# Optimization experiments

Hardware: AMD Instinct MI355X
Metric: run time of the kernel (lower is better)

The kernel has to match this reference:

```python
import jax, jax.numpy as jnp
import numpy as np

V, E, H, B, S = 32000, 512, 1024, 128, 512
NEG = -1e9


def setup_inputs() -> dict:
    key = jax.random.key(0)
    ks = jax.random.split(key, 12)
    s = 0.02
    return {
        "previous_word": jax.random.randint(ks[0], (B, 1), 0, V),
        "h_0": jax.random.normal(ks[1], (B, H), jnp.float32),
        "c_0": jax.random.normal(ks[2], (B, H), jnp.float32),
        "ctx": jax.random.normal(ks[3], (B, S, H), jnp.float32),
        "ctx_mask": jnp.zeros((B, S), dtype=bool),
        "emb": jax.random.normal(ks[4], (V, E), jnp.float32) * s,
        "W_ih": jax.random.normal(ks[5], (4 * H, E), jnp.float32) * s,
        "W_hh": jax.random.normal(ks[6], (4 * H, H), jnp.float32) * s,
        "b_ih": jnp.zeros((4 * H,), jnp.float32),
        "b_hh": jnp.zeros((4 * H,), jnp.float32),
        "W_in": jax.random.normal(ks[7], (H, H), jnp.float32) * s,
        "W_out": jax.random.normal(ks[8], (H, 2 * H), jnp.float32) * s,
        "W_dec": jax.random.normal(ks[9], (V, H), jnp.float32) * s,
        "b_dec": jnp.zeros((V,), jnp.float32),
    }


def reference(previous_word, h_0, c_0, ctx, ctx_mask, emb, W_ih, W_hh, b_ih, b_hh, W_in, W_out, W_dec, b_dec):
    # embedding lookup + squeeze; dropout is identity in eval mode
    x = emb[previous_word[:, 0]]                       # [B, E]
    # LSTMCell: gate order i, f, g, o (PyTorch convention)
    gates = x @ W_ih.T + b_ih + h_0 @ W_hh.T + b_hh    # [B, 4H]
    i, f, g, o = jnp.split(gates, 4, axis=1)
    i = jax.nn.sigmoid(i)
    f = jax.nn.sigmoid(f)
    g = jnp.tanh(g)
    o = jax.nn.sigmoid(o)
    c_1 = f * c_0 + i * g
    h_1 = o * jnp.tanh(c_1)
    # SoftDotAttention
    target = h_1 @ W_in.T                               # [B, H]
    attn = jnp.einsum('bsh,bh->bs', ctx, target)        # [B, S]
    attn = jnp.where(ctx_mask, NEG, attn)
    alpha = jax.nn.softmax(attn, axis=1)
    weighted = jnp.einsum('bs,bsh->bh', alpha, ctx)     # [B, H]
    h_tilde = jnp.tanh(jnp.concatenate([weighted, h_1], axis=1) @ W_out.T)
    logit = h_tilde @ W_dec.T + b_dec                   # [B, V]
    return (h_1, c_1, alpha, logit)
```

## Files before the change

kernel.cpp:

```cpp
#include <hip/hip_runtime.h>
#include <hip/hip_bf16.h>
#include <cstdint>

#define NEG_BIG (-1.0e9f)

typedef __attribute__((ext_vector_type(8))) short short8_t;
typedef __attribute__((ext_vector_type(4))) float f32x4;

typedef __attribute__((address_space(1))) const unsigned int gu32_t;
typedef __attribute__((address_space(3))) unsigned int lu32_t;

__device__ __forceinline__ short f2bf(float x) {
  union { float f; unsigned u; } v; v.f = x;
  unsigned r = v.u + 0x7fffu + ((v.u >> 16) & 1u);
  return (short)(r >> 16);
}
__device__ __forceinline__ float sigmoidf_(float x) { return 1.0f / (1.0f + __expf(-x)); }

__device__ __forceinline__ void lds_barrier() {
  asm volatile("s_waitcnt lgkmcnt(0)\n\ts_barrier" ::: "memory");
}
__device__ __forceinline__ void block_barrier() {
  asm volatile("" ::: "memory");
  __builtin_amdgcn_s_barrier();
  asm volatile("" ::: "memory");
}

__launch_bounds__(256, 2)
__global__ void k_gates(const int* __restrict__ prev, const float* __restrict__ emb,
                        const float* __restrict__ h0,
                        const float* __restrict__ W_ih, const float* __restrict__ W_hh,
                        const float* __restrict__ b_ih, const float* __restrict__ b_hh,
                        const float* __restrict__ c0,
                        float* __restrict__ h1_out, float* __restrict__ c1_out,
                        short* __restrict__ A3) {
  __shared__ __align__(16) short lA[2][64 * 64];
  __shared__ __align__(16) short lW[2][64 * 64];
  const int tid = threadIdx.x;
  const int wid = tid >> 6, l = tid & 63, l15 = l & 15, khalf = l >> 4;
  const int hb = blockIdx.x;
  const int mrow0 = blockIdx.y * 64;

  const int arow = tid >> 2;
  const int apart = tid & 3;
  const int aswz = (arow & 7) << 4;
  const int bA = mrow0 + arow;
  const int pv = prev[bA];
  const float* embrow = emb + (size_t)pv * 512 + apart * 16;
  const float* h0row = h0 + (size_t)bA * 1024 + apart * 16;

  int wrow_[4], wkq_[4];
  const float* wih_[4];
  const float* whh_[4];
#pragma unroll
  for (int j = 0; j < 4; ++j) {
    int idx = j * 1024 + tid * 4;
    int n = idx >> 6;
    wkq_[j] = idx & 63;
    wrow_[j] = n;
    int grow = (n >> 4) * 1024 + hb * 16 + (n & 15);
    wih_[j] = W_ih + (size_t)grow * 512;
    whh_[j] = W_hh + (size_t)grow * 1024;
  }

  f32x4 acc[4];
#pragma unroll
  for (int r = 0; r < 4; ++r) acc[r] = (f32x4){0.f, 0.f, 0.f, 0.f};

  float4 aF[4], wR[4];
  auto stage_regs = [&](int k0) {
    const float* asrc = (k0 < 512) ? (embrow + k0) : (h0row + (k0 - 512));
#pragma unroll
    for (int q = 0; q < 4; ++q) aF[q] = *(const float4*)(asrc + q * 4);
#pragma unroll
    for (int j = 0; j < 4; ++j) {
      int kg = k0 + wkq_[j];
      wR[j] = (kg < 512) ? *(const float4*)(wih_[j] + kg)
                         : *(const float4*)(whh_[j] + (kg - 512));
    }
  };
  auto write_lds = [&](int buf) {
    char* drow = (char*)lA[buf] + arow * 128;
#pragma unroll
    for (int q = 0; q < 2; ++q) {
      short8_t s;
      s[0] = f2bf(aF[2 * q].x); s[1] = f2bf(aF[2 * q].y);
      s[2] = f2bf(aF[2 * q].z); s[3] = f2bf(aF[2 * q].w);
      s[4] = f2bf(aF[2 * q + 1].x); s[5] = f2bf(aF[2 * q + 1].y);
      s[6] = f2bf(aF[2 * q + 1].z); s[7] = f2bf(aF[2 * q + 1].w);
      *(short8_t*)(drow + ((apart * 32 + q * 16) ^ aswz)) = s;
    }
#pragma unroll
    for (int j = 0; j < 4; ++j) {
      short4 h4;
      h4.x = f2bf(wR[j].x); h4.y = f2bf(wR[j].y); h4.z = f2bf(wR[j].z); h4.w = f2bf(wR[j].w);
      *(short4*)((char*)lW[buf] + wrow_[j] * 128 + ((wkq_[j] * 2) ^ ((wrow_[j] & 7) << 4))) = h4;
    }
  };
  auto compute = [&](int buf) {
#pragma unroll
    for (int ks = 0; ks < 2; ++ks) {
      const int ubyte = ks * 64 + khalf * 16;
      const int nrow = wid * 16 + l15;
      short8_t bfrag = *(const short8_t*)((char*)lW[buf] + nrow * 128 + (ubyte ^ ((nrow & 7) << 4)));
#pragma unroll
      for (int r = 0; r < 4; ++r) {
        const int mrow = r * 16 + l15;
        short8_t afrag = *(const short8_t*)((char*)lA[buf] + mrow * 128 + (ubyte ^ ((mrow & 7) << 4)));
        acc[r] = __builtin_amdgcn_mfma_f32_16x16x32_bf16(afrag, bfrag, acc[r], 0, 0, 0);
      }
    }
  };

  stage_regs(0);
  write_lds(0);
  for (int t = 0; t < 24; ++t) {
    const int cur = t & 1;
    if (t + 1 < 24) stage_regs((t + 1) << 6);
    lds_barrier();
    compute(cur);
    if (t + 1 < 24) write_lds(cur ^ 1);
  }

  lds_barrier();
  float* gbuf = (float*)&lA[0][0];
#pragma unroll
  for (int r = 0; r < 4; ++r)
#pragma unroll
    for (int e = 0; e < 4; ++e)
      gbuf[wid * 1024 + (r * 16 + khalf * 4 + e) * 16 + l15] = acc[r][e];
  __syncthreads();
#pragma unroll
  for (int q = 0; q < 4; ++q) {
    int idx = q * 256 + tid;
    int hloc = idx & 15, mloc = idx >> 4;
    int b = mrow0 + mloc;
    int hh = hb * 16 + hloc;
    float iv = gbuf[0 + mloc * 16 + hloc] + b_ih[hh] + b_hh[hh];
    float fv = gbuf[1024 + mloc * 16 + hloc] + b_ih[1024 + hh] + b_hh[1024 + hh];
    float gv = gbuf[2048 + mloc * 16 + hloc] + b_ih[2048 + hh] + b_hh[2048 + hh];
    float ov = gbuf[3072 + mloc * 16 + hloc] + b_ih[3072 + hh] + b_hh[3072 + hh];
    float c1 = sigmoidf_(fv) * c0[(size_t)b * 1024 + hh] + sigmoidf_(iv) * tanhf(gv);
    float h1 = sigmoidf_(ov) * tanhf(c1);
    c1_out[(size_t)b * 1024 + hh] = c1;
    h1_out[(size_t)b * 1024 + hh] = h1;
    A3[(size_t)b * 2048 + 1024 + hh] = f2bf(h1);
  }
}

template <int MB, int WN, int EPI>
__launch_bounds__(256, 2)
__global__ void k_gemm(const short* __restrict__ A, int lda,
                       const float* __restrict__ Wa, int ldwa, int Ka,
                       const float* __restrict__ Wb, int ldwb, int Ktot,
                       const float* __restrict__ bias0, const float* __restrict__ bias1,
                       float* __restrict__ outF, short* __restrict__ outB, int ldo,
                       int kstride, size_t pstride) {
  constexpr int BN = WN * 16;
  constexpr int MREP = (MB == 128) ? 2 * WN : 1;
  constexpr int AU = MB / 32;
  constexpr int WLOADS = (BN * 64) / 1024;
  __shared__ __align__(16) short lA[2][MB * 64];
  __shared__ __align__(16) short lW[2][BN * 64];
  const int kc = blockIdx.z;
  A += (size_t)kc * kstride;
  Wa += (size_t)kc * kstride;
  if (outF) outF += (size_t)kc * pstride;
  const int tid = threadIdx.x;
  const int wid = tid >> 6, l = tid & 63, l15 = l & 15, khalf = l >> 4;
  const int nblk = blockIdx.x;
  const int mrow0 = blockIdx.y * MB;
  const int m_wave = (WN == 1) ? wid * (MB / 4) : 0;
  const int nb_local = (WN == 4) ? wid * 16 : 0;

  const int arow = (MB == 128) ? (tid >> 1) : (tid >> 2);
  const int apart = (MB == 128) ? (tid & 1) : (tid & 3);
  const int abase = apart * (AU * 16);
  const int aswz = (arow & 7) << 4;
  const short* Arow = A + (size_t)(mrow0 + arow) * lda + apart * (AU * 8);

  int wn_[WLOADS], wkq_[WLOADS];
#pragma unroll
  for (int j = 0; j < WLOADS; ++j) {
    int idx = j * 1024 + tid * 4;
    wn_[j] = idx >> 6;
    wkq_[j] = idx & 63;
  }

  f32x4 acc[MREP];
#pragma unroll
  for (int r = 0; r < MREP; ++r) acc[r] = (f32x4){0.f, 0.f, 0.f, 0.f};

  short8_t aR[AU];
  float4 wR[WLOADS];

  auto stage_regs = [&](int k0) {
#pragma unroll
    for (int q = 0; q < AU; ++q) aR[q] = *(const short8_t*)(Arow + k0 + q * 8);
#pragma unroll
    for (int j = 0; j < WLOADS; ++j) {
      int kg = k0 + wkq_[j];
      const float* p = (kg < Ka) ? (Wa + (size_t)(nblk * BN + wn_[j]) * ldwa + kg)
                                 : (Wb + (size_t)(nblk * BN + wn_[j]) * ldwb + (kg - Ka));
      wR[j] = *(const float4*)p;
    }
  };
  auto write_lds = [&](int buf) {
    char* drow = (char*)lA[buf] + arow * 128;
#pragma unroll
    for (int q = 0; q < AU; ++q)
      *(short8_t*)(drow + ((abase + q * 16) ^ aswz)) = aR[q];
#pragma unroll
    for (int j = 0; j < WLOADS; ++j) {
      short4 h4;
      h4.x = f2bf(wR[j].x); h4.y = f2bf(wR[j].y); h4.z = f2bf(wR[j].z); h4.w = f2bf(wR[j].w);
      *(short4*)((char*)lW[buf] + wn_[j] * 128 + ((wkq_[j] * 2) ^ ((wn_[j] & 7) << 4))) = h4;
    }
  };
  auto compute = [&](int buf) {
#pragma unroll
    for (int ks = 0; ks < 2; ++ks) {
      const int ubyte = ks * 64 + khalf * 16;
      const int nrow = nb_local + l15;
      short8_t bfrag = *(const short8_t*)((char*)lW[buf] + nrow * 128 + (ubyte ^ ((nrow & 7) << 4)));
#pragma unroll
      for (int r = 0; r < MREP; ++r) {
        const int mrow = m_wave + r * 16 + l15;
        short8_t afrag = *(const short8_t*)((char*)lA[buf] + mrow * 128 + (ubyte ^ ((mrow & 7) << 4)));
        acc[r] = __builtin_amdgcn_mfma_f32_16x16x32_bf16(afrag, bfrag, acc[r], 0, 0, 0);
      }
    }
  };

  const int NT = Ktot >> 6;
  stage_regs(0);
  write_lds(0);
  for (int t = 0; t < NT; ++t) {
    const int cur = t & 1;
    if (t + 1 < NT) stage_regs((t + 1) << 6);
    lds_barrier();
    compute(cur);
    if (t + 1 < NT) write_lds(cur ^ 1);
  }

  const int n = nblk * BN + nb_local + l15;
  float bias = 0.f;
  if (bias0) bias = bias0[n];
  if (bias1) bias += bias1[n];
#pragma unroll
  for (int r = 0; r < MREP; ++r) {
    int mb = mrow0 + m_wave + r * 16 + khalf * 4;
#pragma unroll
    for (int e = 0; e < 4; ++e) {
      float v = acc[r][e] + bias;
      if (EPI == 1) {
        outB[(size_t)(mb + e) * ldo + n] = f2bf(tanhf(v));
      } else {
        outF[(size_t)(mb + e) * ldo + n] = v;
      }
    }
  }
}

__launch_bounds__(256, 2)
__global__ void k_attn(const float* __restrict__ ctx, const float* __restrict__ tp,
                       const unsigned char* __restrict__ mask,
                       float* __restrict__ scores, float* __restrict__ part) {
  __shared__ __align__(16) float lds[2][8 * 1024];
  __shared__ float sml[8];
  const int b = blockIdx.x >> 2, chunk = blockIdx.x & 3;
  const int tid = threadIdx.x;
  const int wid = tid >> 6, l = tid & 63;
  float4 t4[4], w4[4];
#pragma unroll
  for (int j = 0; j < 4; ++j) {
    float4 a = {0.f, 0.f, 0.f, 0.f};
#pragma unroll
    for (int p = 0; p < 4; ++p) {
      const float4 v = *(const float4*)(tp + (size_t)p * 131072 + (size_t)b * 1024 + j * 256 + l * 4);
      a.x += v.x; a.y += v.y; a.z += v.z; a.w += v.w;
    }
    t4[j] = a;
    w4[j].x = 0.f; w4[j].y = 0.f; w4[j].z = 0.f; w4[j].w = 0.f;
  }
  float m = -INFINITY, lsum = 0.f;
  const int s0 = chunk * 128;
  const float* cb = ctx + ((size_t)b * 512 + s0) * 1024;
  const unsigned char* mk = mask + (size_t)b * 512 + s0;

  auto stage = [&](int buf, int tt) {
    const char* src = (const char*)(cb + (size_t)tt * 8192);
    char* dst = (char*)&lds[buf][0];
#pragma unroll
    for (int i = 0; i < 8; ++i) {
      const int off = i * 4096 + tid * 16;
      __builtin_amdgcn_global_load_lds((gu32_t*)(src + off), (lu32_t*)(dst + off), 16, 0, 0);
    }
  };

  stage(0, 0);
  int buf = 0;
  for (int t = 0; t < 16; ++t) {
    if (t < 15) {
      stage(buf ^ 1, t + 1);
      asm volatile("s_waitcnt vmcnt(8)" ::: "memory");
    } else {
      asm volatile("s_waitcnt vmcnt(0)" ::: "memory");
    }
    block_barrier();
#pragma unroll
    for (int rr = 0; rr < 2; ++rr) {
      const int r = wid * 2 + rr;
      const float* row = &lds[buf][r * 1024];
      float4 c0 = *(const float4*)(row + l * 4);
      float4 c1 = *(const float4*)(row + 256 + l * 4);
      float4 c2 = *(const float4*)(row + 512 + l * 4);
      float4 c3 = *(const float4*)(row + 768 + l * 4);
      float p = c0.x * t4[0].x + c0.y * t4[0].y + c0.z * t4[0].z + c0.w * t4[0].w +
                c1.x * t4[1].x + c1.y * t4[1].y + c1.z * t4[1].z + c1.w * t4[1].w +
                c2.x * t4[2].x + c2.y * t4[2].y + c2.z * t4[2].z + c2.w * t4[2].w +
                c3.x * t4[3].x + c3.y * t4[3].y + c3.z * t4[3].z + c3.w * t4[3].w;
#pragma unroll
      for (int off = 32; off > 0; off >>= 1) p += __shfl_xor(p, off);
      const int sg = t * 8 + r;
      if (mk[sg]) p = NEG_BIG;
      if (l == 0) scores[(size_t)b * 512 + s0 + sg] = p;
      float mn = fmaxf(m, p);
      float scale = __expf(m - mn);
      float e = __expf(p - mn);
      lsum = lsum * scale + e;
      w4[0].x = w4[0].x * scale + e * c0.x; w4[0].y = w4[0].y * scale + e * c0.y;
      w4[0].z = w4[0].z * scale + e * c0.z; w4[0].w = w4[0].w * scale + e * c0.w;
      w4[1].x = w4[1].x * scale + e * c1.x; w4[1].y = w4[1].y * scale + e * c1.y;
      w4[1].z = w4[1].z * scale + e * c1.z; w4[1].w = w4[1].w * scale + e * c1.w;
      w4[2].x = w4[2].x * scale + e * c2.x; w4[2].y = w4[2].y * scale + e * c2.y;
      w4[2].z = w4[2].z * scale + e * c2.z; w4[2].w = w4[2].w * scale + e * c2.w;
      w4[3].x = w4[3].x * scale + e * c3.x; w4[3].y = w4[3].y * scale + e * c3.y;
      w4[3].z = w4[3].z * scale + e * c3.z; w4[3].w = w4[3].w * scale + e * c3.w;
      m = mn;
    }
    block_barrier();
    buf ^= 1;
  }

  float* cbuf = &lds[0][0];
#pragma unroll
  for (int j = 0; j < 4; ++j) *(float4*)(cbuf + wid * 1024 + j * 256 + l * 4) = w4[j];
  if (l == 0) { sml[wid] = m; sml[4 + wid] = lsum; }
  __syncthreads();
  const float M = fmaxf(fmaxf(sml[0], sml[1]), fmaxf(sml[2], sml[3]));
  const float sc0 = __expf(sml[0] - M), sc1 = __expf(sml[1] - M);
  const float sc2 = __expf(sml[2] - M), sc3 = __expf(sml[3] - M);
  const float L = sml[4] * sc0 + sml[5] * sc1 + sml[6] * sc2 + sml[7] * sc3;
  const float4 v0 = *(const float4*)(cbuf + 0 * 1024 + tid * 4);
  const float4 v1 = *(const float4*)(cbuf + 1 * 1024 + tid * 4);
  const float4 v2 = *(const float4*)(cbuf + 2 * 1024 + tid * 4);
  const float4 v3 = *(const float4*)(cbuf + 3 * 1024 + tid * 4);
  float4 o;
  o.x = v0.x * sc0 + v1.x * sc1 + v2.x * sc2 + v3.x * sc3;
  o.y = v0.y * sc0 + v1.y * sc1 + v2.y * sc2 + v3.y * sc3;
  o.z = v0.z * sc0 + v1.z * sc1 + v2.z * sc2 + v3.z * sc3;
  o.w = v0.w * sc0 + v1.w * sc1 + v2.w * sc2 + v3.w * sc3;
  float* pp = part + ((size_t)b * 4 + chunk) * 1028;
  *(float4*)(pp + tid * 4) = o;
  if (tid == 0) { pp[1024] = M; pp[1025] = L; }
}

__launch_bounds__(256, 2)
__global__ void k_wgemm(const short* __restrict__ A3, const float* __restrict__ part,
                        const float* __restrict__ W_out, float* __restrict__ wp) {
  __shared__ __align__(16) short lA[2][128 * 64];
  __shared__ __align__(16) short lW[2][16 * 64];
  const int kc = blockIdx.z, nblk = blockIdx.x;
  const int tid = threadIdx.x;
  const int wid = tid >> 6, l = tid & 63, l15 = l & 15, khalf = l >> 4;
  const int arow = tid >> 1, apart = tid & 1;
  const int aswz = (arow & 7) << 4;
  const bool wpath = (kc < 4);

  const int colbase = kc * 256 + apart * 32;
  const short* ArowB = A3 + (size_t)arow * 2048 + colbase;
  const float* ps = part + (size_t)arow * 4 * 1028;
  const float* pr0 = ps + colbase;
  const float* pr1 = ps + 1028 + colbase;
  const float* pr2 = ps + 2056 + colbase;
  const float* pr3 = ps + 3084 + colbase;
  float coef0 = 0.f, coef1 = 0.f, coef2 = 0.f, coef3 = 0.f;
  if (wpath) {
    float m0 = ps[1024], l0 = ps[1025], m1 = ps[1028 + 1024], l1 = ps[1028 + 1025];
    float m2 = ps[2056 + 1024], l2 = ps[2056 + 1025], m3 = ps[3084 + 1024], l3 = ps[3084 + 1025];
    float M = fmaxf(fmaxf(m0, m1), fmaxf(m2, m3));
    float s0 = __expf(m0 - M), s1 = __expf(m1 - M), s2 = __expf(m2 - M), s3 = __expf(m3 - M);
    float inv = 1.0f / (l0 * s0 + l1 * s1 + l2 * s2 + l3 * s3);
    coef0 = s0 * inv; coef1 = s1 * inv; coef2 = s2 * inv; coef3 = s3 * inv;
  }

  const int wn = (tid * 4) >> 6, wkq = (tid * 4) & 63;
  const float* wrow = W_out + (size_t)(nblk * 16 + wn) * 2048 + kc * 256;

  f32x4 acc[2];
  acc[0] = (f32x4){0.f, 0.f, 0.f, 0.f};
  acc[1] = (f32x4){0.f, 0.f, 0.f, 0.f};
  float4 aC[8];
  short8_t aB[4];
  float4 wR;

  auto stage_regs = [&](int k0) {
    if (wpath) {
#pragma unroll
      for (int q = 0; q < 8; ++q) {
        const float4 v0 = *(const float4*)(pr0 + k0 + q * 4);
        const float4 v1 = *(const float4*)(pr1 + k0 + q * 4);
        const float4 v2 = *(const float4*)(pr2 + k0 + q * 4);
        const float4 v3 = *(const float4*)(pr3 + k0 + q * 4);
        aC[q].x = coef0 * v0.x + coef1 * v1.x + coef2 * v2.x + coef3 * v3.x;
        aC[q].y = coef0 * v0.y + coef1 * v1.y + coef2 * v2.y + coef3 * v3.y;
        aC[q].z = coef0 * v0.z + coef1 * v1.z + coef2 * v2.z + coef3 * v3.z;
        aC[q].w = coef0 * v0.w + coef1 * v1.w + coef2 * v2.w + coef3 * v3.w;
      }
    } else {
#pragma unroll
      for (int q = 0; q < 4; ++q) aB[q] = *(const short8_t*)(ArowB + k0 + q * 8);
    }
    wR = *(const float4*)(wrow + k0 + wkq);
  };
  auto write_lds = [&](int buf) {
    char* drow = (char*)lA[buf] + arow * 128;
    if (wpath) {
#pragma unroll
      for (int q2 = 0; q2 < 4; ++q2) {
        short8_t s;
        s[0] = f2bf(aC[2 * q2].x); s[1] = f2bf(aC[2 * q2].y);
        s[2] = f2bf(aC[2 * q2].z); s[3] = f2bf(aC[2 * q2].w);
        s[4] = f2bf(aC[2 * q2 + 1].x); s[5] = f2bf(aC[2 * q2 + 1].y);
        s[6] = f2bf(aC[2 * q2 + 1].z); s[7] = f2bf(aC[2 * q2 + 1].w);
        *(short8_t*)(drow + ((apart * 64 + q2 * 16) ^ aswz)) = s;
      }
    } else {
#pragma unroll
      for (int q = 0; q < 4; ++q)
        *(short8_t*)(drow + ((apart * 64 + q * 16) ^ aswz)) = aB[q];
    }
    short4 h4;
    h4.x = f2bf(wR.x); h4.y = f2bf(wR.y); h4.z = f2bf(wR.z); h4.w = f2bf(wR.w);
    *(short4*)((char*)lW[buf] + wn * 128 + ((wkq * 2) ^ ((wn & 7) << 4))) = h4;
  };
  auto compute = [&](int buf) {
#pragma unroll
    for (int ks = 0; ks < 2; ++ks) {
      const int ubyte = ks * 64 + khalf * 16;
      short8_t bfrag = *(const short8_t*)((char*)lW[buf] + l15 * 128 + (ubyte ^ ((l15 & 7) << 4)));
#pragma unroll
      for (int r = 0; r < 2; ++r) {
        const int mrow = wid * 32 + r * 16 + l15;
        short8_t afrag = *(const short8_t*)((char*)lA[buf] + mrow * 128 + (ubyte ^ ((mrow & 7) << 4)));
        acc[r] = __builtin_amdgcn_mfma_f32_16x16x32_bf16(afrag, bfrag, acc[r], 0, 0, 0);
      }
    }
  };

  stage_regs(0);
  write_lds(0);
  for (int t = 0; t < 4; ++t) {
    const int cur = t & 1;
    if (t + 1 < 4) stage_regs((t + 1) << 6);
    lds_barrier();
    compute(cur);
    if (t + 1 < 4) write_lds(cur ^ 1);
  }

  const int n = nblk * 16 + l15;
  float* out = wp + (size_t)kc * 131072;
#pragma unroll
  for (int r = 0; r < 2; ++r) {
    int mb = wid * 32 + r * 16 + khalf * 4;
#pragma unroll
    for (int e = 0; e < 4; ++e)
      out[(size_t)(mb + e) * 1024 + n] = acc[r][e];
  }
}

__global__ void k_fin2(const float* __restrict__ wp, const float* __restrict__ part,
                       const float* __restrict__ scores, short* __restrict__ ht,
                       float* __restrict__ alpha) {
  int t = blockIdx.x * 256 + threadIdx.x;
  float s = 0.f;
#pragma unroll
  for (int p = 0; p < 8; ++p) s += wp[(size_t)p * 131072 + t];
  ht[t] = f2bf(tanhf(s));
  if (t < 65536) {
    int b = t >> 9, si = t & 511;
    const float* ps = part + (size_t)b * 4 * 1028;
    float m0 = ps[1024], l0 = ps[1025], m1 = ps[1028 + 1024], l1 = ps[1028 + 1025];
    float m2 = ps[2056 + 1024], l2 = ps[2056 + 1025], m3 = ps[3084 + 1024], l3 = ps[3084 + 1025];
    float M = fmaxf(fmaxf(m0, m1), fmaxf(m2, m3));
    float L = l0 * __expf(m0 - M) + l1 * __expf(m1 - M) + l2 * __expf(m2 - M) +
              l3 * __expf(m3 - M);
    alpha[t] = __expf(scores[(size_t)b * 512 + si] - M) / L;
  }
}

extern "C" void kernel_launch(void* const* d_in, const int* in_sizes, int n_in,
                              void* d_out, int out_size, void* d_ws, size_t ws_size,
                              hipStream_t stream) {
  const int* prev = (const int*)d_in[0];
  const float* h0 = (const float*)d_in[1];
  const float* c0 = (const float*)d_in[2];
  const float* ctx = (const float*)d_in[3];
  const unsigned char* mask = (const unsigned char*)d_in[4];
  const float* emb = (const float*)d_in[5];
  const float* W_ih = (const float*)d_in[6];
  const float* W_hh = (const float*)d_in[7];
  const float* b_ih = (const float*)d_in[8];
  const float* b_hh = (const float*)d_in[9];
  const float* W_in = (const float*)d_in[10];
  const float* W_out = (const float*)d_in[11];
  const float* W_dec = (const float*)d_in[12];
  const float* b_dec = (const float*)d_in[13];

  float* out_h1 = (float*)d_out;
  float* out_c1 = out_h1 + 128 * 1024;
  float* out_alpha = out_c1 + 128 * 1024;
  float* out_logit = out_alpha + 128 * 512;

  char* ws = (char*)d_ws;
  short* A3 = (short*)(ws + 0x000000);
  float* scores = (float*)(ws + 0x100000);
  float* tp = (float*)(ws + 0x200000);
  float* part = (float*)(ws + 0x400000);
  float* wp = (float*)(ws + 0x700000);
  short* htilde = (short*)(ws + 0xB00000);

  k_gates<<<dim3(64, 2), 256, 0, stream>>>(prev, emb, h0, W_ih, W_hh, b_ih, b_hh, c0,
                                           out_h1, out_c1, A3);
  k_gemm<128, 1, 0><<<dim3(64, 1, 4), 256, 0, stream>>>(
      A3 + 1024, 2048, W_in, 1024, 1 << 30, W_in, 1024, 256, nullptr, nullptr, tp, nullptr,
      1024, 256, (size_t)131072);
  k_attn<<<512, 256, 0, stream>>>(ctx, tp, mask, scores, part);
  k_wgemm<<<dim3(64, 1, 8), 256, 0, stream>>>(A3, part, W_out, wp);
  k_fin2<<<512, 256, 0, stream>>>(wp, part, scores, htilde, out_alpha);
  k_gemm<128, 4, 0><<<dim3(500, 1, 1), 256, 0, stream>>>(
      htilde, 1024, W_dec, 1024, 1024, W_dec, 1024, 1024, b_dec, nullptr, out_logit, nullptr,
      32000, 0, 0);
}
```

Baseline: 144.1 us.

## Split fused LSTM gate kernel into pack, generic GEMM, and pointwise kernels

Replaces the fused k_gates kernel, which ran on a 64x2 grid, with three steps. A packing kernel writes the bf16 [emb|h0] activations, the generic k_gemm then runs over 256 blocks to produce fp32 gates, and a pointwise LSTM kernel computes c1 and h1. The goal is to spread the gate GEMM across more blocks and CUs so the weight streaming parallelises better. In exchange it adds two extra launches and round-trips the gates and the packed activations through global memory.

```diff
diff --git a/kernel.cpp b/kernel.cpp
--- a/kernel.cpp
+++ b/kernel.cpp
@@ -26,126 +26,13 @@
   asm volatile("" ::: "memory");
 }
 
-__launch_bounds__(256, 2)
-__global__ void k_gates(const int* __restrict__ prev, const float* __restrict__ emb,
-                        const float* __restrict__ h0,
-                        const float* __restrict__ W_ih, const float* __restrict__ W_hh,
-                        const float* __restrict__ b_ih, const float* __restrict__ b_hh,
-                        const float* __restrict__ c0,
-                        float* __restrict__ h1_out, float* __restrict__ c1_out,
-                        short* __restrict__ A3) {
-  __shared__ __align__(16) short lA[2][64 * 64];
-  __shared__ __align__(16) short lW[2][64 * 64];
-  const int tid = threadIdx.x;
-  const int wid = tid >> 6, l = tid & 63, l15 = l & 15, khalf = l >> 4;
-  const int hb = blockIdx.x;
-  const int mrow0 = blockIdx.y * 64;
-
-  const int arow = tid >> 2;
-  const int apart = tid & 3;
-  const int aswz = (arow & 7) << 4;
-  const int bA = mrow0 + arow;
-  const int pv = prev[bA];
-  const float* embrow = emb + (size_t)pv * 512 + apart * 16;
-  const float* h0row = h0 + (size_t)bA * 1024 + apart * 16;
-
-  int wrow_[4], wkq_[4];
-  const float* wih_[4];
-  const float* whh_[4];
-#pragma unroll
-  for (int j = 0; j < 4; ++j) {
-    int idx = j * 1024 + tid * 4;
-    int n = idx >> 6;
-    wkq_[j] = idx & 63;
-    wrow_[j] = n;
-    int grow = (n >> 4) * 1024 + hb * 16 + (n & 15);
-    wih_[j] = W_ih + (size_t)grow * 512;
-    whh_[j] = W_hh + (size_t)grow * 1024;
-  }
-
-  f32x4 acc[4];
-#pragma unroll
-  for (int r = 0; r < 4; ++r) acc[r] = (f32x4){0.f, 0.f, 0.f, 0.f};
-
-  float4 aF[4], wR[4];
-  auto stage_regs = [&](int k0) {
-    const float* asrc = (k0 < 512) ? (embrow + k0) : (h0row + (k0 - 512));
-#pragma unroll
-    for (int q = 0; q < 4; ++q) aF[q] = *(const float4*)(asrc + q * 4);
-#pragma unroll
-    for (int j = 0; j < 4; ++j) {
-      int kg = k0 + wkq_[j];
-      wR[j] = (kg < 512) ? *(const float4*)(wih_[j] + kg)
-                         : *(const float4*)(whh_[j] + (kg - 512));
-    }
-  };
-  auto write_lds = [&](int buf) {
-    char* drow = (char*)lA[buf] + arow * 128;
-#pragma unroll
-    for (int q = 0; q < 2; ++q) {
-      short8_t s;
-      s[0] = f2bf(aF[2 * q].x); s[1] = f2bf(aF[2 * q].y);
-      s[2] = f2bf(aF[2 * q].z); s[3] = f2bf(aF[2 * q].w);
-      s[4] = f2bf(aF[2 * q + 1].x); s[5] = f2bf(aF[2 * q + 1].y);
-      s[6] = f2bf(aF[2 * q + 1].z); s[7] = f2bf(aF[2 * q + 1].w);
-      *(short8_t*)(drow + ((apart * 32 + q * 16) ^ aswz)) = s;
-    }
-#pragma unroll
-    for (int j = 0; j < 4; ++j) {
-      short4 h4;
-      h4.x = f2bf(wR[j].x); h4.y = f2bf(wR[j].y); h4.z = f2bf(wR[j].z); h4.w = f2bf(wR[j].w);
-      *(short4*)((char*)lW[buf] + wrow_[j] * 128 + ((wkq_[j] * 2) ^ ((wrow_[j] & 7) << 4))) = h4;
-    }
-  };
-  auto compute = [&](int buf) {
-#pragma unroll
-    for (int ks = 0; ks < 2; ++ks) {
-      const int ubyte = ks * 64 + khalf * 16;
-      const int nrow = wid * 16 + l15;
-      short8_t bfrag = *(const short8_t*)((char*)lW[buf] + nrow * 128 + (ubyte ^ ((nrow & 7) << 4)));
-#pragma unroll
-      for (int r = 0; r < 4; ++r) {
-        const int mrow = r * 16 + l15;
-        short8_t afrag = *(const short8_t*)((char*)lA[buf] + mrow * 128 + (ubyte ^ ((mrow & 7) << 4)));
-        acc[r] = __builtin_amdgcn_mfma_f32_16x16x32_bf16(afrag, bfrag, acc[r], 0, 0, 0);
-      }
-    }
-  };
-
-  stage_regs(0);
-  write_lds(0);
-  for (int t = 0; t < 24; ++t) {
-    const int cur = t & 1;
-    if (t + 1 < 24) stage_regs((t + 1) << 6);
-    lds_barrier();
-    compute(cur);
-    if (t + 1 < 24) write_lds(cur ^ 1);
-  }
-
-  lds_barrier();
-  float* gbuf = (float*)&lA[0][0];
-#pragma unroll
-  for (int r = 0; r < 4; ++r)
-#pragma unroll
-    for (int e = 0; e < 4; ++e)
-      gbuf[wid * 1024 + (r * 16 + khalf * 4 + e) * 16 + l15] = acc[r][e];
-  __syncthreads();
-#pragma unroll
-  for (int q = 0; q < 4; ++q) {
-    int idx = q * 256 + tid;
-    int hloc = idx & 15, mloc = idx >> 4;
-    int b = mrow0 + mloc;
-    int hh = hb * 16 + hloc;
-    float iv = gbuf[0 + mloc * 16 + hloc] + b_ih[hh] + b_hh[hh];
-    float fv = gbuf[1024 + mloc * 16 + hloc] + b_ih[1024 + hh] + b_hh[1024 + hh];
-    float gv = gbuf[2048 + mloc * 16 + hloc] + b_ih[2048 + hh] + b_hh[2048 + hh];
-    float ov = gbuf[3072 + mloc * 16 + hloc] + b_ih[3072 + hh] + b_hh[3072 + hh];
-    float c1 = sigmoidf_(fv) * c0[(size_t)b * 1024 + hh] + sigmoidf_(iv) * tanhf(gv);
-    float h1 = sigmoidf_(ov) * tanhf(c1);
-    c1_out[(size_t)b * 1024 + hh] = c1;
-    h1_out[(size_t)b * 1024 + hh] = h1;
-    A3[(size_t)b * 2048 + 1024 + hh] = f2bf(h1);
-  }
+__global__ void k_pack_a1(const int* __restrict__ prev, const float* __restrict__ emb,
+                          const float* __restrict__ h0, short* __restrict__ A1) {
+  int t = blockIdx.x * 256 + threadIdx.x;
+  if (t >= 128 * 1536) return;
+  int b = t / 1536, k = t - b * 1536;
+  float v = (k < 512) ? emb[(size_t)prev[b] * 512 + k] : h0[b * 1024 + (k - 512)];
+  A1[t] = f2bf(v);
 }
 
 template <int MB, int WN, int EPI>
@@ -262,6 +149,23 @@
   }
 }
 
+__global__ void k_lstm(const float* __restrict__ gates, const float* __restrict__ c0,
+                       float* __restrict__ h1_out, float* __restrict__ c1_out,
+                       short* __restrict__ A3) {
+  int t = blockIdx.x * 256 + threadIdx.x;
+  int b = t >> 10, h = t & 1023;
+  const float* g = gates + (size_t)b * 4096;
+  float ig = sigmoidf_(g[h]);
+  float fg = sigmoidf_(g[1024 + h]);
+  float gg = tanhf(g[2048 + h]);
+  float og = sigmoidf_(g[3072 + h]);
+  float c1 = fg * c0[t] + ig * gg;
+  float h1 = og * tanhf(c1);
+  c1_out[t] = c1;
+  h1_out[t] = h1;
+  A3[(size_t)b * 2048 + 1024 + h] = f2bf(h1);
+}
+
 __launch_bounds__(256, 2)
 __global__ void k_attn(const float* __restrict__ ctx, const float* __restrict__ tp,
                        const unsigned char* __restrict__ mask,
@@ -529,10 +433,14 @@
   float* tp = (float*)(ws + 0x200000);
   float* part = (float*)(ws + 0x400000);
   float* wp = (float*)(ws + 0x700000);
-  short* htilde = (short*)(ws + 0xB00000);
-
-  k_gates<<<dim3(64, 2), 256, 0, stream>>>(prev, emb, h0, W_ih, W_hh, b_ih, b_hh, c0,
-                                           out_h1, out_c1, A3);
+  float* gates = (float*)(ws + 0xB00000);
+  short* A1 = (short*)(ws + 0xD00000);
+  short* htilde = (short*)(ws + 0xE00000);
+
+  k_pack_a1<<<768, 256, 0, stream>>>(prev, emb, h0, A1);
+  k_gemm<128, 1, 0><<<dim3(256, 1, 1), 256, 0, stream>>>(
+      A1, 1536, W_ih, 512, 512, W_hh, 1024, 1536, b_ih, b_hh, gates, nullptr, 4096, 0, 0);
+  k_lstm<<<512, 256, 0, stream>>>(gates, c0, out_h1, out_c1, A3);
   k_gemm<128, 1, 0><<<dim3(64, 1, 4), 256, 0, stream>>>(
       A3 + 1024, 2048, W_in, 1024, 1 << 30, W_in, 1024, 256, nullptr, nullptr, tp, nullptr,
       1024, 256, (size_t)131072);
```

New measurement: 146.5 us. About the same (+1.7%).
